# Kernel tuning notes

Measured on AMD Instinct MI355X. Metric: run time of the kernel, lower is better.

The kernel has to match this reference:

```python
import jax, jax.numpy as jnp
import numpy as np

B, T, H = 32, 512, 512
NUM_LAYERS = 2  # outer modules; each nn.GRU itself has NUM_LAYERS internal layers
TOTAL = NUM_LAYERS * NUM_LAYERS  # 4 actual recurrent layers
EPS = 1e-5


def setup_inputs() -> dict:
    key = jax.random.key(0)
    ks = jax.random.split(key, 8)
    s = 1.0 / np.sqrt(H)
    x = jax.random.normal(ks[0], (B, T, H), dtype=jnp.float32)
    # descending lengths in [1, T] (enforce_sorted=True in torch)
    seq_lens = jnp.sort(jax.random.randint(ks[1], (B,), 1, T + 1))[::-1]
    Wih = jax.random.uniform(ks[2], (TOTAL, 3 * H, H), minval=-s, maxval=s)
    Whh = jax.random.uniform(ks[3], (TOTAL, 3 * H, H), minval=-s, maxval=s)
    bih = jax.random.uniform(ks[4], (TOTAL, 3 * H), minval=-s, maxval=s)
    bhh = jax.random.uniform(ks[5], (TOTAL, 3 * H), minval=-s, maxval=s)
    gamma = jnp.ones((NUM_LAYERS, H), jnp.float32)
    beta = jnp.zeros((NUM_LAYERS, H), jnp.float32)
    return {"x": x, "Wih": Wih, "Whh": Whh, "bih": bih, "bhh": bhh,
            "gamma": gamma, "beta": beta, "seq_lens": seq_lens}


def _gru_layer(x, wih, whh, bi, bh):
    # x: [B,T,I]; torch GRU equations (gate order r,z,n)
    xi = jnp.einsum('bti,gi->btg', x, wih) + bi  # [B,T,3H]

    def step(h, xt):
        hh = h @ whh.T + bh
        xr, xz, xn = jnp.split(xt, 3, axis=-1)
        hr, hz, hn = jnp.split(hh, 3, axis=-1)
        r = jax.nn.sigmoid(xr + hr)
        z = jax.nn.sigmoid(xz + hz)
        n = jnp.tanh(xn + r * hn)
        h = (1 - z) * n + z * h
        return h, h

    h0 = jnp.zeros((x.shape[0], whh.shape[1]), x.dtype)
    _, ys = jax.lax.scan(step, h0, jnp.swapaxes(xi, 0, 1))  # [T,B,H]
    return jnp.swapaxes(ys, 0, 1)


def _layernorm(x, g, b):
    mu = jnp.mean(x, axis=-1, keepdims=True)
    var = jnp.mean(jnp.square(x - mu), axis=-1, keepdims=True)
    return (x - mu) * jax.lax.rsqrt(var + EPS) * g + b


def reference(x, Wih, Whh, bih, bhh, gamma, beta, seq_lens):
    # pack_padded_sequence semantics (unidirectional): outputs at valid steps
    # t < len match the full-sequence run; padded steps become zeros after
    # pad_packed_sequence, then LayerNorm is applied to the whole padded tensor.
    mask = (jnp.arange(T)[None, :] < seq_lens[:, None])[:, :, None]  # [B,T,1]
    out = x
    idx = 0
    for l in range(NUM_LAYERS):
        for _k in range(NUM_LAYERS):  # each nn.GRU has NUM_LAYERS internal layers
            out = _gru_layer(out, Wih[idx], Whh[idx], bih[idx], bhh[idx])
            idx += 1
        out = jnp.where(mask, out, 0.0)
        out = _layernorm(out, gamma[l], beta[l])
    return out
```

## Files before the change

### kernel.cpp

```cpp
#include <hip/hip_runtime.h>

typedef unsigned short ushort_t;
typedef __attribute__((ext_vector_type(8))) short short8;
typedef __attribute__((ext_vector_type(4))) float f32x4;

#define B_ 32
#define T_ 512
#define H_ 512
#define CH_ 16

__device__ __forceinline__ float bf2f(ushort_t u) {
  union { unsigned int i; float f; } v; v.i = ((unsigned int)u) << 16; return v.f;
}
__device__ __forceinline__ ushort_t f2bf(float f) {
  union { float fv; unsigned int i; } v; v.fv = f;
  unsigned int x = v.i;
  x += 0x7fffu + ((x >> 16) & 1u);
  return (ushort_t)(x >> 16);
}

__device__ __forceinline__ float fsig(float a) {
  return __builtin_amdgcn_rcpf(1.f + __expf(-a));
}
__device__ __forceinline__ float ftanh(float a) {
  return 1.f - 2.f * __builtin_amdgcn_rcpf(1.f + __expf(2.f * a));
}

__device__ __forceinline__ void cload16(short8& dst, const ushort_t* p) {
  asm volatile("global_load_dwordx4 %0, %1, off sc0 sc1"
               : "=v"(dst) : "v"(p) : "memory");
}
__device__ __forceinline__ void cstore16(const short8& v, ushort_t* p) {
  asm volatile("global_store_dwordx4 %1, %0, off sc0 sc1"
               :: "v"(v), "v"(p) : "memory");
}
#define WAIT_VM0 asm volatile("s_waitcnt vmcnt(0)" ::: "memory")
__device__ __forceinline__ void vfence(short8& v) { asm volatile("" : "+v"(v)); }

__device__ __forceinline__ void poll_row(const int* row, int nf) {
  const int lane = threadIdx.x & 63;
  if (nf > 64) {
    for (;;) {
      int a = __hip_atomic_load(row + lane,      __ATOMIC_RELAXED, __HIP_MEMORY_SCOPE_AGENT);
      int b = __hip_atomic_load(row + 64 + lane, __ATOMIC_RELAXED, __HIP_MEMORY_SCOPE_AGENT);
      if (__all(a != 0 && b != 0)) break;
      __builtin_amdgcn_s_sleep(1);
    }
  } else {
    for (;;) {
      int a = (lane < nf)
            ? __hip_atomic_load(row + lane, __ATOMIC_RELAXED, __HIP_MEMORY_SCOPE_AGENT) : 1;
      if (__all(a != 0)) break;
      __builtin_amdgcn_s_sleep(1);
    }
  }
  asm volatile("" ::: "memory");
}

__global__ void prep_w(const float* __restrict__ Wih, const float* __restrict__ Whh,
                       ushort_t* __restrict__ WihBf, ushort_t* __restrict__ WhhBf) {
  int i = blockIdx.x * 256 + threadIdx.x;
  WihBf[i] = f2bf(Wih[i]);
  WhhBf[i] = f2bf(Whh[i]);
}
__global__ void prep_x(const float* __restrict__ x, ushort_t* __restrict__ xA) {
  int i = blockIdx.x * 256 + threadIdx.x;
  int h  = i & (H_ - 1);
  int tb = i >> 9;
  int b  = tb & (B_ - 1);
  int t  = tb >> 5;
  xA[i] = f2bf(x[((size_t)b * T_ + t) * H_ + h]);
}

__device__ void gru_stage(
    const ushort_t* __restrict__ xin, ushort_t* __restrict__ xout,
    const ushort_t* __restrict__ Wih, const ushort_t* __restrict__ Whh,
    const float* __restrict__ bih, const float* __restrict__ bhh,
    ushort_t* __restrict__ hbuf,
    int* __restrict__ selfFl,
    const int* __restrict__ prodFl,
    int prodN, int wg,
    float (*Gbuf)[2][48][33])
{
  const int tid   = threadIdx.x;
  const int lane  = tid & 63;
  const int wave  = tid >> 6;
  const int jb    = wg * CH_;
  const int m16   = lane & 15;
  const int quad  = lane >> 4;
  const int bcol  = (wave & 1) * 16 + m16;

  const ushort_t* Wsel = (wave < 2) ? Wih : Whh;
  short8 afrag[3][16];
#pragma unroll
  for (int g = 0; g < 3; ++g) {
    const ushort_t* wp = Wsel + (size_t)(g * H_ + jb + m16) * H_ + quad * 8;
#pragma unroll
    for (int kk = 0; kk < 16; ++kk)
      afrag[g][kk] = *(const short8*)(wp + kk * 32);
  }

  const int b0 = tid & 31;
  const int c  = tid >> 5;
  const int c0 = 2 * c, c1 = 2 * c + 1;
  const float bxr0 = bih[0*H_ + jb + c0], bhr0 = bhh[0*H_ + jb + c0];
  const float bxz0 = bih[1*H_ + jb + c0], bhz0 = bhh[1*H_ + jb + c0];
  const float bxn0 = bih[2*H_ + jb + c0], bhn0 = bhh[2*H_ + jb + c0];
  const float bxr1 = bih[0*H_ + jb + c1], bhr1 = bhh[0*H_ + jb + c1];
  const float bxz1 = bih[1*H_ + jb + c1], bhz1 = bhh[1*H_ + jb + c1];
  const float bxn1 = bih[2*H_ + jb + c1], bhn1 = bhh[2*H_ + jb + c1];
  float hp0 = 0.f, hp1 = 0.f;

  for (int s = 0; s < T_; ++s) {
    const int p = s & 1;
    f32x4 acc0 = {0.f, 0.f, 0.f, 0.f};
    f32x4 acc1 = acc0, acc2 = acc0;

    if (wave < 2) {
      const ushort_t* src = xin + ((size_t)s * B_ + bcol) * H_ + quad * 8;
      if (prodFl) {
        poll_row(prodFl + s * prodN, prodN);
        short8 bfr[16];
#pragma unroll
        for (int kk = 0; kk < 16; ++kk) cload16(bfr[kk], src + kk * 32);
        WAIT_VM0;
#pragma unroll
        for (int kk = 0; kk < 16; ++kk) {
          vfence(bfr[kk]);
          acc0 = __builtin_amdgcn_mfma_f32_16x16x32_bf16(afrag[0][kk], bfr[kk], acc0, 0, 0, 0);
          acc1 = __builtin_amdgcn_mfma_f32_16x16x32_bf16(afrag[1][kk], bfr[kk], acc1, 0, 0, 0);
          acc2 = __builtin_amdgcn_mfma_f32_16x16x32_bf16(afrag[2][kk], bfr[kk], acc2, 0, 0, 0);
        }
      } else {
#pragma unroll
        for (int kk = 0; kk < 16; ++kk) {
          short8 bf = *(const short8*)(src + kk * 32);
          acc0 = __builtin_amdgcn_mfma_f32_16x16x32_bf16(afrag[0][kk], bf, acc0, 0, 0, 0);
          acc1 = __builtin_amdgcn_mfma_f32_16x16x32_bf16(afrag[1][kk], bf, acc1, 0, 0, 0);
          acc2 = __builtin_amdgcn_mfma_f32_16x16x32_bf16(afrag[2][kk], bf, acc2, 0, 0, 0);
        }
      }
    } else {
      if (s > 0) poll_row(selfFl + (s - 1) * 128, 128);
      const ushort_t* src = hbuf + ((size_t)p * B_ + bcol) * H_ + quad * 8;
      short8 bfr[16];
#pragma unroll
      for (int kk = 0; kk < 16; ++kk) cload16(bfr[kk], src + kk * 32);
      WAIT_VM0;
#pragma unroll
      for (int kk = 0; kk < 16; ++kk) {
        vfence(bfr[kk]);
        acc0 = __builtin_amdgcn_mfma_f32_16x16x32_bf16(afrag[0][kk], bfr[kk], acc0, 0, 0, 0);
        acc1 = __builtin_amdgcn_mfma_f32_16x16x32_bf16(afrag[1][kk], bfr[kk], acc1, 0, 0, 0);
        acc2 = __builtin_amdgcn_mfma_f32_16x16x32_bf16(afrag[2][kk], bfr[kk], acc2, 0, 0, 0);
      }
    }

    float (*Gd)[33] = Gbuf[p][(wave < 2) ? 0 : 1];
#pragma unroll
    for (int r = 0; r < 4; ++r) {
      Gd[ 0 + quad * 4 + r][bcol] = acc0[r];
      Gd[16 + quad * 4 + r][bcol] = acc1[r];
      Gd[32 + quad * 4 + r][bcol] = acc2[r];
    }
    __syncthreads();

    float (*Gx)[33] = Gbuf[p][0];
    float (*Gh)[33] = Gbuf[p][1];
    ushort_t* hdst = hbuf + (size_t)(p ^ 1) * B_ * H_;
    {
      float rr = fsig(Gx[c0][b0] + bxr0 + Gh[c0][b0] + bhr0);
      float zz = fsig(Gx[16 + c0][b0] + bxz0 + Gh[16 + c0][b0] + bhz0);
      float nn = ftanh(Gx[32 + c0][b0] + bxn0 + rr * (Gh[32 + c0][b0] + bhn0));
      hp0 = (1.f - zz) * nn + zz * hp0;
    }
    {
      float rr = fsig(Gx[c1][b0] + bxr1 + Gh[c1][b0] + bhr1);
      float zz = fsig(Gx[16 + c1][b0] + bxz1 + Gh[16 + c1][b0] + bhz1);
      float nn = ftanh(Gx[32 + c1][b0] + bxn1 + rr * (Gh[32 + c1][b0] + bhn1));
      hp1 = (1.f - zz) * nn + zz * hp1;
    }
    unsigned int pack = (unsigned int)f2bf(hp0) | ((unsigned int)f2bf(hp1) << 16);
    __hip_atomic_store((unsigned int*)(hdst + (size_t)b0 * H_ + jb + c0), pack,
                       __ATOMIC_RELAXED, __HIP_MEMORY_SCOPE_AGENT);
    __hip_atomic_store((unsigned int*)(xout + ((size_t)s * B_ + b0) * H_ + jb + c0), pack,
                       __ATOMIC_RELAXED, __HIP_MEMORY_SCOPE_AGENT);

    WAIT_VM0;
    if (lane == 0)
      __hip_atomic_store(selfFl + s * 128 + wg * 4 + wave, 1,
                         __ATOMIC_RELAXED, __HIP_MEMORY_SCOPE_AGENT);
  }
}

__device__ void ln_stage(
    const ushort_t* __restrict__ xin,
    ushort_t* __restrict__ xout_bf,
    float* __restrict__ out_f32,
    const float* __restrict__ gamma, const float* __restrict__ beta,
    const int* __restrict__ seq,
    int* __restrict__ selfFl,
    const int* __restrict__ prodFl, int prodN, int wg)
{
  const int lane = threadIdx.x & 63;
  const int wv   = threadIdx.x >> 6;
  const int b    = wg * 4 + wv;
  const int len  = seq[b];
  const int h0   = lane * 8;

  float g[8], be[8];
#pragma unroll
  for (int j = 0; j < 8; ++j) { g[j] = gamma[h0 + j]; be[j] = beta[h0 + j]; }

  for (int s = 0; s < T_; ++s) {
    poll_row(prodFl + s * prodN, prodN);
    short8 raw;
    cload16(raw, xin + ((size_t)s * B_ + b) * H_ + h0);
    WAIT_VM0;
    vfence(raw);
    const bool valid = s < len;
    float v[8];
#pragma unroll
    for (int j = 0; j < 8; ++j) v[j] = valid ? bf2f((ushort_t)raw[j]) : 0.f;

    float sum = 0.f, sq = 0.f;
#pragma unroll
    for (int j = 0; j < 8; ++j) { sum += v[j]; sq += v[j] * v[j]; }
#pragma unroll
    for (int off = 32; off > 0; off >>= 1) {
      sum += __shfl_xor(sum, off);
      sq  += __shfl_xor(sq, off);
    }
    float mu   = sum * (1.f / H_);
    float var  = sq * (1.f / H_) - mu * mu;
    float rstd = rsqrtf(var + 1e-5f);

    if (xout_bf) {
      short8 o;
#pragma unroll
      for (int j = 0; j < 8; ++j)
        o[j] = (short)f2bf((v[j] - mu) * rstd * g[j] + be[j]);
      cstore16(o, xout_bf + ((size_t)s * B_ + b) * H_ + h0);
      WAIT_VM0;
      if (lane == 0)
        __hip_atomic_store(selfFl + s * 32 + b, 1,
                           __ATOMIC_RELAXED, __HIP_MEMORY_SCOPE_AGENT);
    } else {
      float* dst = out_f32 + ((size_t)b * T_ + s) * H_ + h0;
#pragma unroll
      for (int j = 0; j < 8; ++j)
        dst[j] = (v[j] - mu) * rstd * g[j] + be[j];
    }
  }
}

__global__ __launch_bounds__(256, 1) void gru_mega(
    ushort_t* __restrict__ xA, ushort_t* __restrict__ xB, ushort_t* __restrict__ xC,
    const ushort_t* __restrict__ WihBf, const ushort_t* __restrict__ WhhBf,
    const float* __restrict__ bih, const float* __restrict__ bhh,
    const float* __restrict__ gamma, const float* __restrict__ beta,
    const int* __restrict__ seq,
    ushort_t* __restrict__ hbase, int* __restrict__ flbase,
    float* __restrict__ out)
{
  __shared__ float Gbuf[2][2][48][33];

  const int bid = blockIdx.x;
  const int GRUF = T_ * 128;
  const int LNF  = T_ * 32;
  int* fl0   = flbase;
  int* fl1   = flbase + GRUF;
  int* flln0 = flbase + 2 * GRUF;
  int* fl2   = flbase + 2 * GRUF + LNF;
  int* fl3   = flbase + 3 * GRUF + LNF;
  const int WM  = 3 * H_ * H_;
  const int HBL = 2 * B_ * H_;

  if (bid < 32) {
    gru_stage(xA, xB, WihBf, WhhBf, bih, bhh,
              hbase, fl0, nullptr, 0, bid, Gbuf);
  } else if (bid < 64) {
    gru_stage(xB, xC, WihBf + WM, WhhBf + WM, bih + 1536, bhh + 1536,
              hbase + HBL, fl1, fl0, 128, bid - 32, Gbuf);
  } else if (bid < 72) {
    ln_stage(xC, xA, nullptr, gamma, beta, seq, flln0, fl1, 128, bid - 64);
  } else if (bid < 104) {
    gru_stage(xA, xC, WihBf + 2 * WM, WhhBf + 2 * WM, bih + 2 * 1536, bhh + 2 * 1536,
              hbase + 2 * HBL, fl2, flln0, 32, bid - 72, Gbuf);
  } else if (bid < 136) {
    gru_stage(xC, xB, WihBf + 3 * WM, WhhBf + 3 * WM, bih + 3 * 1536, bhh + 3 * 1536,
              hbase + 3 * HBL, fl3, fl2, 128, bid - 104, Gbuf);
  } else {
    ln_stage(xB, nullptr, out, gamma + H_, beta + H_, seq,
             nullptr, fl3, 128, bid - 136);
  }
}

#define WIH_OFF 0u
#define WHH_OFF 6291456u
#define XA_OFF  12582912u
#define XB_OFF  29360128u
#define XC_OFF  46137344u
#define HB_OFF  62914560u
#define FL_OFF  63176704u

extern "C" void kernel_launch(void* const* d_in, const int* in_sizes, int n_in,
                              void* d_out, int out_size, void* d_ws, size_t ws_size,
                              hipStream_t stream) {
  (void)in_sizes; (void)n_in; (void)out_size; (void)ws_size;
  const float* x     = (const float*)d_in[0];
  const float* Wih   = (const float*)d_in[1];
  const float* Whh   = (const float*)d_in[2];
  const float* bih   = (const float*)d_in[3];
  const float* bhh   = (const float*)d_in[4];
  const float* gamma = (const float*)d_in[5];
  const float* beta  = (const float*)d_in[6];
  const int*   seq   = (const int*)d_in[7];

  char* ws = (char*)d_ws;
  ushort_t* WihBf = (ushort_t*)(ws + WIH_OFF);
  ushort_t* WhhBf = (ushort_t*)(ws + WHH_OFF);
  ushort_t* xA    = (ushort_t*)(ws + XA_OFF);
  ushort_t* xB    = (ushort_t*)(ws + XB_OFF);
  ushort_t* xC    = (ushort_t*)(ws + XC_OFF);
  ushort_t* hbase = (ushort_t*)(ws + HB_OFF);
  int*      flags = (int*)(ws + FL_OFF);

  hipMemsetAsync(ws + HB_OFF, 0, 262144u + 1114112u, stream);

  prep_w<<<3145728 / 256, 256, 0, stream>>>(Wih, Whh, WihBf, WhhBf);
  prep_x<<<8388608 / 256, 256, 0, stream>>>(x, xA);

  gru_mega<<<144, 256, 0, stream>>>(xA, xB, xC, WihBf, WhhBf,
                                    bih, bhh, gamma, beta, seq,
                                    hbase, flags, (float*)d_out);
}
```

Before: 3.890 ms.

## Interleave stage-to-block mapping and add a cross-block handshake barrier

Block IDs are remapped so each stage takes blocks with a fixed residue mod 8, with 256 blocks launched and the extra ones exiting at once. The likely aim is to place blocks of one GRU stage across XCDs or CUs in a chosen pattern, for better cache locality or co-residency. The GRU blocks also run a spin handshake through new flag memory that checks all 32 blocks of each stage are resident. Its result is written to a status flag that nothing reads yet. This adds startup latency and spin traffic, and timeouts guard against deadlock.

```diff
diff --git a/kernel.cpp b/kernel.cpp
--- a/kernel.cpp
+++ b/kernel.cpp
@@ -265,7 +265,12 @@
 {
   __shared__ float Gbuf[2][2][48][33];
 
-  const int bid = blockIdx.x;
+  const int bid  = blockIdx.x;
+  const int r8   = bid & 7;
+  const int slot = bid >> 3;
+  if (r8 >= 6) return;
+  if (r8 >= 4 && slot >= 8) return;
+
   const int GRUF = T_ * 128;
   const int LNF  = T_ * 32;
   int* fl0   = flbase;
@@ -273,26 +278,62 @@
   int* flln0 = flbase + 2 * GRUF;
   int* fl2   = flbase + 2 * GRUF + LNF;
   int* fl3   = flbase + 3 * GRUF + LNF;
+  int* hsk   = flbase + 4 * GRUF + LNF;
   const int WM  = 3 * H_ * H_;
   const int HBL = 2 * B_ * H_;
 
-  if (bid < 32) {
+  if (r8 < 4) {
+    if (threadIdx.x < 64) {
+      const int lane = threadIdx.x;
+      int* t = hsk + r8 * 32;
+      int* o = hsk + 128 + r8 * 32;
+      int ok = 1;
+      for (int round = 1; round <= 2 && ok; ++round) {
+        if (lane == 0) *(volatile int*)(t + slot) = round;
+        int it = 0;
+        for (;;) {
+          int v;
+          asm volatile("global_load_dword %0, %1, off sc0\n\ts_waitcnt vmcnt(0)"
+                       : "=&v"(v) : "v"(t + (lane & 31)) : "memory");
+          if (__all(v >= round && v <= 2)) break;
+          if (++it > 512) { ok = 0; break; }
+        }
+      }
+      if (lane == 0)
+        __hip_atomic_store(o + slot, ok + 1,
+                           __ATOMIC_RELAXED, __HIP_MEMORY_SCOPE_AGENT);
+      int v2 = 0, it2 = 0;
+      for (;;) {
+        v2 = __hip_atomic_load(o + (lane & 31),
+                               __ATOMIC_RELAXED, __HIP_MEMORY_SCOPE_AGENT);
+        if (__all(v2 != 0)) break;
+        if (++it2 > 100000) break;
+        __builtin_amdgcn_s_sleep(1);
+      }
+      if (lane == 0)
+        __hip_atomic_store(hsk + 256 + r8, __all(v2 == 2) ? 1 : 0,
+                           __ATOMIC_RELAXED, __HIP_MEMORY_SCOPE_AGENT);
+    }
+    __syncthreads();
+  }
+
+  if (r8 == 0) {
     gru_stage(xA, xB, WihBf, WhhBf, bih, bhh,
-              hbase, fl0, nullptr, 0, bid, Gbuf);
-  } else if (bid < 64) {
+              hbase, fl0, nullptr, 0, slot, Gbuf);
+  } else if (r8 == 1) {
     gru_stage(xB, xC, WihBf + WM, WhhBf + WM, bih + 1536, bhh + 1536,
-              hbase + HBL, fl1, fl0, 128, bid - 32, Gbuf);
-  } else if (bid < 72) {
-    ln_stage(xC, xA, nullptr, gamma, beta, seq, flln0, fl1, 128, bid - 64);
-  } else if (bid < 104) {
+              hbase + HBL, fl1, fl0, 128, slot, Gbuf);
+  } else if (r8 == 2) {
     gru_stage(xA, xC, WihBf + 2 * WM, WhhBf + 2 * WM, bih + 2 * 1536, bhh + 2 * 1536,
-              hbase + 2 * HBL, fl2, flln0, 32, bid - 72, Gbuf);
-  } else if (bid < 136) {
+              hbase + 2 * HBL, fl2, flln0, 32, slot, Gbuf);
+  } else if (r8 == 3) {
     gru_stage(xC, xB, WihBf + 3 * WM, WhhBf + 3 * WM, bih + 3 * 1536, bhh + 3 * 1536,
-              hbase + 3 * HBL, fl3, fl2, 128, bid - 104, Gbuf);
+              hbase + 3 * HBL, fl3, fl2, 128, slot, Gbuf);
+  } else if (r8 == 4) {
+    ln_stage(xC, xA, nullptr, gamma, beta, seq, flln0, fl1, 128, slot);
   } else {
     ln_stage(xB, nullptr, out, gamma + H_, beta + H_, seq,
-             nullptr, fl3, 128, bid - 136);
+             nullptr, fl3, 128, slot);
   }
 }
 
@@ -326,12 +367,12 @@
   ushort_t* hbase = (ushort_t*)(ws + HB_OFF);
   int*      flags = (int*)(ws + FL_OFF);
 
-  hipMemsetAsync(ws + HB_OFF, 0, 262144u + 1114112u, stream);
+  hipMemsetAsync(ws + HB_OFF, 0, 1377312u, stream);
 
   prep_w<<<3145728 / 256, 256, 0, stream>>>(Wih, Whh, WihBf, WhhBf);
   prep_x<<<8388608 / 256, 256, 0, stream>>>(x, xA);
 
-  gru_mega<<<144, 256, 0, stream>>>(xA, xB, xC, WihBf, WhhBf,
+  gru_mega<<<256, 256, 0, stream>>>(xA, xB, xC, WihBf, WhhBf,
                                     bih, bhh, gamma, beta, seq,
                                     hbase, flags, (float*)d_out);
 }
```

New measurement: 4.661 ms. 1.2x slower.
